# Optimization experiments

Measured on AMD Instinct MI355X. Metric: run time of the kernel, lower is better.

Reference implementation:

```python
import jax, jax.numpy as jnp
import numpy as np
import math

D_MODEL = 1024
NUM_HEADS = 16
D_K = D_MODEL // NUM_HEADS
B, S = 2, 2048


def _linear_weight(key, out_f, in_f):
    return jax.random.normal(key, (out_f, in_f), jnp.float32) * math.sqrt(2.0 / in_f)


def setup_inputs() -> dict:
    key = jax.random.key(0)
    ks = jax.random.split(key, 5)
    x = jax.random.normal(ks[0], (B, S, D_MODEL), jnp.float32)
    return {
        "x": x,
        "Wq": _linear_weight(ks[1], D_MODEL, D_MODEL),
        "bq": jnp.zeros((D_MODEL,), jnp.float32),
        "Wk": _linear_weight(ks[2], D_MODEL, D_MODEL),
        "bk": jnp.zeros((D_MODEL,), jnp.float32),
        "Wv": _linear_weight(ks[3], D_MODEL, D_MODEL),
        "bv": jnp.zeros((D_MODEL,), jnp.float32),
        "Wo": _linear_weight(ks[4], D_MODEL, D_MODEL),
        "bo": jnp.zeros((D_MODEL,), jnp.float32),
    }


def reference(x, Wq, bq, Wk, bk, Wv, bv, Wo, bo):
    b, s, _ = x.shape
    # Projections: x @ W.T + b (CustomLinear stores weight as (out, in))
    q = jnp.einsum("bsd,ed->bse", x, Wq) + bq
    k = jnp.einsum("bsd,ed->bse", x, Wk) + bk
    v = jnp.einsum("bsd,ed->bse", x, Wv) + bv
    # (b, h, s, d_k)
    q = q.reshape(b, s, NUM_HEADS, D_K).transpose(0, 2, 1, 3)
    k = k.reshape(b, s, NUM_HEADS, D_K).transpose(0, 2, 1, 3)
    v = v.reshape(b, s, NUM_HEADS, D_K).transpose(0, 2, 1, 3)
    # Scaled dot-product attention with fully materialized scores (faithful)
    scores = jnp.einsum("bhqd,bhkd->bhqk", q, k) / math.sqrt(D_K)
    attn = jax.nn.softmax(scores, axis=-1)
    out = jnp.einsum("bhqk,bhkd->bhqd", attn, v)
    out = out.transpose(0, 2, 1, 3).reshape(b, s, D_MODEL)
    return jnp.einsum("bsd,ed->bse", out, Wo) + bo
```

## Files before the change

### kernel.cpp

```cpp
#include <hip/hip_runtime.h>
#include <hip/hip_bf16.h>

using bf16 = __hip_bfloat16;
typedef __attribute__((ext_vector_type(8))) short short8;
typedef __attribute__((ext_vector_type(4))) short s4v;
typedef __attribute__((ext_vector_type(4))) float float4v;
typedef __attribute__((ext_vector_type(4))) float f32x4;
typedef __attribute__((ext_vector_type(16))) float f32x16;
typedef __attribute__((ext_vector_type(4))) int i32x4;

#define MFMA16(a, b, c) __builtin_amdgcn_mfma_f32_16x16x32_bf16((a), (b), (c), 0, 0, 0)
#define MFMA32(a, b, c) __builtin_amdgcn_mfma_f32_32x32x16_bf16((a), (b), (c), 0, 0, 0)

#define GLD_LDS16(g, l)                                            \
    __builtin_amdgcn_global_load_lds(                              \
        (const __attribute__((address_space(1))) void*)(g),        \
        (__attribute__((address_space(3))) void*)(l), 16, 0, 0)

constexpr int Bc = 2;
constexpr int Sc = 2048;
constexpr int Hc = 16;
constexpr int DKc = 64;
constexpr int Dc = 1024;
constexpr size_t MEG = 1024 * 1024;

union BFU { bf16 h; short s; };
union PKU { i32x4 i; short8 s; };

__device__ inline short bfbits(float f) {
    BFU u; u.h = __float2bfloat16(f); return u.s;
}

__device__ inline float bits2f(short s) {
    BFU u; u.s = s; return __bfloat162float(u.h);
}

__device__ inline unsigned cvtpk(float a, float b) {
    unsigned r;
    asm("v_cvt_pk_bf16_f32 %0, %1, %2" : "=v"(r) : "v"(a), "v"(b));
    return r;
}

__device__ inline short8 load_cvt8(const float* __restrict__ p) {
    f32x4 a = *(const f32x4*)p;
    f32x4 b = *(const f32x4*)(p + 4);
    short8 r;
    r[0] = bfbits(a[0]); r[1] = bfbits(a[1]); r[2] = bfbits(a[2]); r[3] = bfbits(a[3]);
    r[4] = bfbits(b[0]); r[5] = bfbits(b[1]); r[6] = bfbits(b[2]); r[7] = bfbits(b[3]);
    return r;
}

__global__ __launch_bounds__(256) void cvt_kernel(
    const float* __restrict__ x, const float* __restrict__ Wq,
    const float* __restrict__ Wk, const float* __restrict__ Wv,
    const float* __restrict__ Wo, bf16* __restrict__ dst)
{
    const size_t i = ((size_t)blockIdx.x * 256 + threadIdx.x) * 8;
    const float* s;
    if      (i < 4 * MEG) s = x  + i;
    else if (i < 5 * MEG) s = Wq + (i - 4 * MEG);
    else if (i < 6 * MEG) s = Wk + (i - 5 * MEG);
    else if (i < 7 * MEG) s = Wv + (i - 6 * MEG);
    else                  s = Wo + (i - 7 * MEG);
    *(short8*)(dst + i) = load_cvt8(s);
}

__global__ __launch_bounds__(256) void qkv_gemm_kernel(
    const bf16* __restrict__ x,
    const bf16* __restrict__ Wq, const float* __restrict__ bq,
    const bf16* __restrict__ Wk, const float* __restrict__ bk,
    const bf16* __restrict__ Wv, const float* __restrict__ bv,
    bf16* __restrict__ q_ws, bf16* __restrict__ k_ws, bf16* __restrict__ v_ws)
{
    constexpr int BM = 128, BN = 128, BK = 32;
    __shared__ __align__(16) bf16 sA[BM * BK];
    __shared__ __align__(16) bf16 sB[BN * BK];

    const int bx = blockIdx.x;
    const int sel = bx >> 3;
    const int n0 = (bx & 7) * BN;
    const int m0 = blockIdx.y * BM;

    const bf16* __restrict__ Wsel = (sel == 0) ? Wq : ((sel == 1) ? Wk : Wv);
    const float* __restrict__ bsel = (sel == 0) ? bq : ((sel == 1) ? bk : bv);

    const int t = threadIdx.x;
    const int lane = t & 63;
    const int wave = t >> 6;
    const int ln = lane & 15;
    const int qd = lane >> 4;
    const int wm = (wave >> 1) * 64;
    const int wn = (wave & 1) * 64;

    const int gr = lane >> 2;
    const int gc = (lane & 3) * 8;

    float4v acc[4][4];
#pragma unroll
    for (int i = 0; i < 4; i++)
#pragma unroll
        for (int j = 0; j < 4; j++) acc[i][j] = (float4v)0.0f;

    for (int kk = 0; kk < Dc; kk += BK) {
        __syncthreads();
#pragma unroll
        for (int cc = 0; cc < 2; cc++) {
            const int c = wave * 2 + cc;
            GLD_LDS16(x    + (size_t)(m0 + c * 16 + gr) * Dc + kk + gc, &sA[c * 512]);
            GLD_LDS16(Wsel + (size_t)(n0 + c * 16 + gr) * Dc + kk + gc, &sB[c * 512]);
        }
        __syncthreads();

        short8 af[4], wf[4];
#pragma unroll
        for (int i = 0; i < 4; i++)
            af[i] = *(const short8*)&sA[(wm + i * 16 + ln) * BK + qd * 8];
#pragma unroll
        for (int j = 0; j < 4; j++)
            wf[j] = *(const short8*)&sB[(wn + j * 16 + ln) * BK + qd * 8];
#pragma unroll
        for (int i = 0; i < 4; i++)
#pragma unroll
            for (int j = 0; j < 4; j++)
                acc[i][j] = MFMA16(af[i], wf[j], acc[i][j]);
    }

    constexpr float QSCALE = 0.125f * 1.44269504088896f;

#pragma unroll
    for (int j = 0; j < 4; j++) {
        const int n = n0 + wn + j * 16 + ln;
        const float bias = bsel[n];
        const int h_ = n >> 6, d_ = n & 63;
#pragma unroll
        for (int i = 0; i < 4; i++) {
            const int mbase = m0 + wm + i * 16 + qd * 4;
            const int b_ = mbase >> 11, s0_ = mbase & 2047;
            if (sel == 2) {
                const int dv_ = d_ >> 5, cV = d_ & 31;
                const int ktg = s0_ >> 6, ksl = (s0_ >> 4) & 3;
                const int hiV = (s0_ >> 3) & 1, i0 = s0_ & 7;
                s4v pk;
#pragma unroll
                for (int r = 0; r < 4; r++)
                    pk[r] = bfbits(acc[i][j][r] + bias);
                *(s4v*)&v_ws[(size_t)(b_ * Hc + h_) * Sc * DKc + ktg * 4096
                             + (dv_ * 4 + ksl) * 512 + (cV + 32 * hiV) * 8 + i0] = pk;
            } else if (sel == 1) {
                const int ks_ = d_ >> 4, hiK = (d_ >> 3) & 1, ii = d_ & 7;
#pragma unroll
                for (int r = 0; r < 4; r++) {
                    const int s_ = s0_ + r;
                    const int ktg = s_ >> 6, kv = (s_ >> 5) & 1, cK = s_ & 31;
                    k_ws[(size_t)(b_ * Hc + h_) * Sc * DKc + ktg * 4096
                         + (kv * 4 + ks_) * 512 + (cK + 32 * hiK) * 8 + ii] =
                        __float2bfloat16(acc[i][j][r] + bias);
                }
            } else {
#pragma unroll
                for (int r = 0; r < 4; r++) {
                    const int s_ = s0_ + r;
                    q_ws[(((size_t)(b_ * Hc + h_)) * Sc + s_) * DKc + d_] =
                        __float2bfloat16((acc[i][j][r] + bias) * QSCALE);
                }
            }
        }
    }
}

__global__ __launch_bounds__(256, 4) void attn_kernel(
    const bf16* __restrict__ q_ws, const bf16* __restrict__ kf_ws,
    const bf16* __restrict__ vf_ws, bf16* __restrict__ po0,
    bf16* __restrict__ po1, float* __restrict__ l_ws)
{
    constexpr int NKT = 16;
    __shared__ __align__(16) bf16 sK[2][8 * 512];
    __shared__ __align__(16) bf16 sV[2][8 * 512];

    const int bh = blockIdx.x;
    const int qt = blockIdx.y;
    const int sp = blockIdx.z;
    const int t = threadIdx.x;
    const int lane = t & 63;
    const int wave = t >> 6;
    const int c = lane & 31;
    const int hi = lane >> 5;

    const bf16* __restrict__ Qbase = q_ws + (size_t)bh * Sc * DKc
                                   + (size_t)(qt * 128 + wave * 32) * DKc;
    const bf16* __restrict__ KF = kf_ws + ((size_t)bh * Sc + sp * 1024) * DKc;
    const bf16* __restrict__ VF = vf_ws + ((size_t)bh * Sc + sp * 1024) * DKc;

    short8 qf[4];
#pragma unroll
    for (int ks = 0; ks < 4; ks++)
        qf[ks] = *(const short8*)(Qbase + (size_t)c * DKc + ks * 16 + hi * 8);

    short8 ones8;
    {
        const short ob = (c == 0) ? (short)0x3F80 : (short)0;
#pragma unroll
        for (int i = 0; i < 8; i++) ones8[i] = ob;
    }

    auto stage = [&](int buf, int kt2) {
#pragma unroll
        for (int cc = 0; cc < 4; cc++) {
            const int cid = (wave << 2) + cc;
            if (cid < 8)
                GLD_LDS16(KF + (size_t)kt2 * 4096 + cid * 512 + lane * 8,
                          &sK[buf][cid * 512]);
            else
                GLD_LDS16(VF + (size_t)kt2 * 4096 + (cid - 8) * 512 + lane * 8,
                          &sV[buf][(cid - 8) * 512]);
        }
    };

    f32x16 oacc0 = (f32x16)0.0f;
    f32x16 oacc1 = (f32x16)0.0f;
    f32x16 den   = (f32x16)0.0f;

    stage(0, 0);

    for (int kt = 0; kt < NKT; kt++) {
        const int cur = kt & 1;
        __syncthreads();
        if (kt + 1 < NKT) stage(cur ^ 1, kt + 1);

#pragma unroll
        for (int kv = 0; kv < 2; kv++) {
            f32x16 sacc = (f32x16)0.0f;
            __builtin_amdgcn_s_setprio(1);
#pragma unroll
            for (int ks = 0; ks < 4; ks++) {
                const short8 kfr = *(const short8*)
                    &sK[cur][(kv * 4 + ks) * 512 + lane * 8];
                sacc = MFMA32(kfr, qf[ks], sacc);
            }
            __builtin_amdgcn_s_setprio(0);

            unsigned s0[4][2], sw[4][2];
#pragma unroll
            for (int q = 0; q < 4; q++)
#pragma unroll
                for (int j = 0; j < 2; j++)
                    s0[q][j] = cvtpk(exp2f(sacc[q * 4 + j * 2]),
                                     exp2f(sacc[q * 4 + j * 2 + 1]));
#pragma unroll
            for (int q = 0; q < 4; q++)
#pragma unroll
                for (int j = 0; j < 2; j++)
                    sw[q][j] = (unsigned)__shfl_xor((int)s0[q][j], 32, 64);

            __builtin_amdgcn_s_setprio(1);
#pragma unroll
            for (int m = 0; m < 2; m++) {
                PKU u;
                u.i[0] = (int)(hi ? sw[2 * m + 1][0] : s0[2 * m][0]);
                u.i[1] = (int)(hi ? sw[2 * m + 1][1] : s0[2 * m][1]);
                u.i[2] = (int)(hi ? s0[2 * m + 1][0] : sw[2 * m][0]);
                u.i[3] = (int)(hi ? s0[2 * m + 1][1] : sw[2 * m][1]);
                const short8 ap = u.s;
                const int ksl = kv * 2 + m;
                const short8 vf0 = *(const short8*)
                    &sV[cur][(0 + ksl) * 512 + lane * 8];
                const short8 vf1 = *(const short8*)
                    &sV[cur][(4 + ksl) * 512 + lane * 8];
                oacc0 = MFMA32(ap, vf0, oacc0);
                oacc1 = MFMA32(ap, vf1, oacc1);
                den   = MFMA32(ap, ones8, den);
            }
            __builtin_amdgcn_s_setprio(0);
        }
    }

    const int b_ = bh >> 4, h_ = bh & 15;
    bf16* __restrict__ po = sp ? po1 : po0;
    if (c == 0) {
#pragma unroll
        for (int r = 0; r < 16; r++) {
            const int qrow = (r & 3) + 8 * (r >> 2) + 4 * hi;
            l_ws[(size_t)(sp * 32 + bh) * Sc + qt * 128 + wave * 32 + qrow] =
                den[r];
        }
    }
#pragma unroll
    for (int r = 0; r < 16; r++) {
        const float l = __shfl(den[r], lane & 32, 64);
        const float inv = 1.0f / l;
        const int qrow = (r & 3) + 8 * (r >> 2) + 4 * hi;
        const int s_ = qt * 128 + wave * 32 + qrow;
        const size_t rowb = (((size_t)(b_ * Sc + s_)) * Hc + h_) * DKc;
        po[rowb + c]      = __float2bfloat16(oacc0[r] * inv);
        po[rowb + 32 + c] = __float2bfloat16(oacc1[r] * inv);
    }
}

__global__ __launch_bounds__(256) void combine_kernel(
    bf16* po0, const bf16* __restrict__ po1, const float* __restrict__ l_ws)
{
    const size_t gid = (size_t)blockIdx.x * 256 + threadIdx.x;
    const size_t e = gid * 8;
    const int flat = (int)(e >> 6);
    const int h_ = flat & 15;
    const int bs = flat >> 4;
    const int b_ = bs >> 11, s_ = bs & 2047;
    const int bh = b_ * Hc + h_;
    const float l0 = l_ws[(size_t)bh * Sc + s_];
    const float l1 = l_ws[(size_t)(32 + bh) * Sc + s_];
    const float inv = 1.0f / (l0 + l1);
    const float w0 = l0 * inv, w1 = l1 * inv;
    const short8 a = *(const short8*)(po0 + e);
    const short8 b = *(const short8*)(po1 + e);
    short8 o;
#pragma unroll
    for (int i = 0; i < 8; i++)
        o[i] = bfbits(bits2f(a[i]) * w0 + bits2f(b[i]) * w1);
    *(short8*)(po0 + e) = o;
}

__global__ __launch_bounds__(256) void out_gemm_kernel(
    const bf16* __restrict__ A, const bf16* __restrict__ Wo,
    const float* __restrict__ bo, float* __restrict__ out)
{
    constexpr int BM = 128, BN = 128, BK = 32;
    __shared__ __align__(16) bf16 sA[BM * BK];
    __shared__ __align__(16) bf16 sB[BN * BK];

    const int n0 = blockIdx.x * BN;
    const int m0 = blockIdx.y * BM;

    const int t = threadIdx.x;
    const int lane = t & 63;
    const int wave = t >> 6;
    const int ln = lane & 15;
    const int qd = lane >> 4;
    const int wm = (wave >> 1) * 64;
    const int wn = (wave & 1) * 64;

    const int gr = lane >> 2;
    const int gc = (lane & 3) * 8;

    float4v acc[4][4];
#pragma unroll
    for (int i = 0; i < 4; i++)
#pragma unroll
        for (int j = 0; j < 4; j++) acc[i][j] = (float4v)0.0f;

    for (int kk = 0; kk < Dc; kk += BK) {
        __syncthreads();
#pragma unroll
        for (int cc = 0; cc < 2; cc++) {
            const int c = wave * 2 + cc;
            GLD_LDS16(A  + (size_t)(m0 + c * 16 + gr) * Dc + kk + gc, &sA[c * 512]);
            GLD_LDS16(Wo + (size_t)(n0 + c * 16 + gr) * Dc + kk + gc, &sB[c * 512]);
        }
        __syncthreads();

        short8 af[4], wf[4];
#pragma unroll
        for (int i = 0; i < 4; i++)
            af[i] = *(const short8*)&sA[(wm + i * 16 + ln) * BK + qd * 8];
#pragma unroll
        for (int j = 0; j < 4; j++)
            wf[j] = *(const short8*)&sB[(wn + j * 16 + ln) * BK + qd * 8];
#pragma unroll
        for (int i = 0; i < 4; i++)
#pragma unroll
            for (int j = 0; j < 4; j++)
                acc[i][j] = MFMA16(af[i], wf[j], acc[i][j]);
    }

#pragma unroll
    for (int j = 0; j < 4; j++) {
        const int n = n0 + wn + j * 16 + ln;
        const float bias = bo[n];
#pragma unroll
        for (int i = 0; i < 4; i++) {
            const int mbase = m0 + wm + i * 16 + qd * 4;
#pragma unroll
            for (int r = 0; r < 4; r++) {
                const int m = mbase + r;
                out[(size_t)m * Dc + n] = acc[i][j][r] + bias;
            }
        }
    }
}

extern "C" void kernel_launch(void* const* d_in, const int* in_sizes, int n_in,
                              void* d_out, int out_size, void* d_ws, size_t ws_size,
                              hipStream_t stream)
{
    const float* x  = (const float*)d_in[0];
    const float* Wq = (const float*)d_in[1];
    const float* bq = (const float*)d_in[2];
    const float* Wk = (const float*)d_in[3];
    const float* bk = (const float*)d_in[4];
    const float* Wv = (const float*)d_in[5];
    const float* bv = (const float*)d_in[6];
    const float* Wo = (const float*)d_in[7];
    const float* bo = (const float*)d_in[8];
    float* out = (float*)d_out;

    bf16* base  = (bf16*)d_ws;
    bf16* q_ws  = base;
    bf16* k_ws  = base + 4 * MEG;
    bf16* v_ws  = base + 8 * MEG;
    bf16* ao_ws = base + 12 * MEG;
    bf16* xb    = base + 16 * MEG;
    bf16* po1   = xb;
    bf16* wqb   = base + 20 * MEG;
    float* l_ws = (float*)wqb;
    bf16* wkb   = base + 21 * MEG;
    bf16* wvb   = base + 22 * MEG;
    bf16* wob   = base + 23 * MEG;

    cvt_kernel<<<dim3(4096), 256, 0, stream>>>(x, Wq, Wk, Wv, Wo, xb);
    qkv_gemm_kernel<<<dim3(24, 32), 256, 0, stream>>>(
        xb, wqb, bq, wkb, bk, wvb, bv, q_ws, k_ws, v_ws);
    attn_kernel<<<dim3(32, 16, 2), 256, 0, stream>>>(
        q_ws, k_ws, v_ws, ao_ws, po1, l_ws);
    combine_kernel<<<dim3(2048), 256, 0, stream>>>(ao_ws, po1, l_ws);
    out_gemm_kernel<<<dim3(8, 32), 256, 0, stream>>>(ao_ws, wob, bo, out);
}
```

Measured before the change: 211.6 us.

## Fuse split-KV combine into output projection GEMM A-tile load

Removes the separate combine kernel. The output GEMM now reads both partial attention outputs and their softmax denominators, forms the weighted sum in registers while staging the A tile into shared memory, and prefetches the next A chunk. The N tile is halved to 64 so the grid doubles, which adds parallelism. In exchange, each block redoes the combine for its rows: A traffic doubles and is repeated across 16 column blocks, and the A loads now go through registers instead of direct global-to-LDS copies.

```diff
diff --git a/kernel.cpp b/kernel.cpp
--- a/kernel.cpp
+++ b/kernel.cpp
@@ -296,34 +296,12 @@
     }
 }
 
-__global__ __launch_bounds__(256) void combine_kernel(
-    bf16* po0, const bf16* __restrict__ po1, const float* __restrict__ l_ws)
-{
-    const size_t gid = (size_t)blockIdx.x * 256 + threadIdx.x;
-    const size_t e = gid * 8;
-    const int flat = (int)(e >> 6);
-    const int h_ = flat & 15;
-    const int bs = flat >> 4;
-    const int b_ = bs >> 11, s_ = bs & 2047;
-    const int bh = b_ * Hc + h_;
-    const float l0 = l_ws[(size_t)bh * Sc + s_];
-    const float l1 = l_ws[(size_t)(32 + bh) * Sc + s_];
-    const float inv = 1.0f / (l0 + l1);
-    const float w0 = l0 * inv, w1 = l1 * inv;
-    const short8 a = *(const short8*)(po0 + e);
-    const short8 b = *(const short8*)(po1 + e);
-    short8 o;
-#pragma unroll
-    for (int i = 0; i < 8; i++)
-        o[i] = bfbits(bits2f(a[i]) * w0 + bits2f(b[i]) * w1);
-    *(short8*)(po0 + e) = o;
-}
-
 __global__ __launch_bounds__(256) void out_gemm_kernel(
-    const bf16* __restrict__ A, const bf16* __restrict__ Wo,
+    const bf16* __restrict__ po0, const bf16* __restrict__ po1,
+    const float* __restrict__ l_ws, const bf16* __restrict__ Wo,
     const float* __restrict__ bo, float* __restrict__ out)
 {
-    constexpr int BM = 128, BN = 128, BK = 32;
+    constexpr int BM = 128, BN = 64, BK = 32;
     __shared__ __align__(16) bf16 sA[BM * BK];
     __shared__ __align__(16) bf16 sB[BN * BK];
 
@@ -336,43 +314,74 @@
     const int ln = lane & 15;
     const int qd = lane >> 4;
     const int wm = (wave >> 1) * 64;
-    const int wn = (wave & 1) * 64;
+    const int wn = (wave & 1) * 32;
 
     const int gr = lane >> 2;
     const int gc = (lane & 3) * 8;
 
-    float4v acc[4][4];
+    const int ar = t >> 2;
+    const int ac = (t & 3) * 8;
+
+    float4v acc[4][2];
 #pragma unroll
     for (int i = 0; i < 4; i++)
 #pragma unroll
-        for (int j = 0; j < 4; j++) acc[i][j] = (float4v)0.0f;
+        for (int j = 0; j < 2; j++) acc[i][j] = (float4v)0.0f;
+
+    short8 a0[2], a1[2];
+    auto loadA = [&](int kk) {
+#pragma unroll
+        for (int L = 0; L < 2; L++) {
+            const size_t row = (size_t)(m0 + L * 64 + ar);
+            a0[L] = *(const short8*)&po0[row * Dc + kk + ac];
+            a1[L] = *(const short8*)&po1[row * Dc + kk + ac];
+        }
+    };
+    loadA(0);
 
     for (int kk = 0; kk < Dc; kk += BK) {
         __syncthreads();
-#pragma unroll
-        for (int cc = 0; cc < 2; cc++) {
-            const int c = wave * 2 + cc;
-            GLD_LDS16(A  + (size_t)(m0 + c * 16 + gr) * Dc + kk + gc, &sA[c * 512]);
-            GLD_LDS16(Wo + (size_t)(n0 + c * 16 + gr) * Dc + kk + gc, &sB[c * 512]);
+        GLD_LDS16(Wo + (size_t)(n0 + wave * 16 + gr) * Dc + kk + gc,
+                  &sB[wave * 512]);
+        const short8 c0_0 = a0[0], c0_1 = a0[1];
+        const short8 c1_0 = a1[0], c1_1 = a1[1];
+        if (kk + BK < Dc) loadA(kk + BK);
+        const int h = kk >> 6;
+#pragma unroll
+        for (int L = 0; L < 2; L++) {
+            const int row = m0 + L * 64 + ar;
+            const int b_ = row >> 11, s_ = row & 2047;
+            const int bhl = b_ * Hc + h;
+            const float l0 = l_ws[(size_t)bhl * Sc + s_];
+            const float l1 = l_ws[(size_t)(32 + bhl) * Sc + s_];
+            const float inv = 1.0f / (l0 + l1);
+            const float w0 = l0 * inv, w1 = l1 * inv;
+            const short8 ca = L ? c0_1 : c0_0;
+            const short8 cb = L ? c1_1 : c1_0;
+            short8 o;
+#pragma unroll
+            for (int e = 0; e < 8; e++)
+                o[e] = bfbits(bits2f(ca[e]) * w0 + bits2f(cb[e]) * w1);
+            *(short8*)&sA[(L * 64 + ar) * BK + ac] = o;
         }
         __syncthreads();
 
-        short8 af[4], wf[4];
+        short8 af[4], wf[2];
 #pragma unroll
         for (int i = 0; i < 4; i++)
             af[i] = *(const short8*)&sA[(wm + i * 16 + ln) * BK + qd * 8];
 #pragma unroll
-        for (int j = 0; j < 4; j++)
+        for (int j = 0; j < 2; j++)
             wf[j] = *(const short8*)&sB[(wn + j * 16 + ln) * BK + qd * 8];
 #pragma unroll
         for (int i = 0; i < 4; i++)
 #pragma unroll
-            for (int j = 0; j < 4; j++)
+            for (int j = 0; j < 2; j++)
                 acc[i][j] = MFMA16(af[i], wf[j], acc[i][j]);
     }
 
 #pragma unroll
-    for (int j = 0; j < 4; j++) {
+    for (int j = 0; j < 2; j++) {
         const int n = n0 + wn + j * 16 + ln;
         const float bias = bo[n];
 #pragma unroll
@@ -420,6 +429,6 @@
         xb, wqb, bq, wkb, bk, wvb, bv, q_ws, k_ws, v_ws);
     attn_kernel<<<dim3(32, 16, 2), 256, 0, stream>>>(
         q_ws, k_ws, v_ws, ao_ws, po1, l_ws);
-    combine_kernel<<<dim3(2048), 256, 0, stream>>>(ao_ws, po1, l_ws);
-    out_gemm_kernel<<<dim3(8, 32), 256, 0, stream>>>(ao_ws, wob, bo, out);
-}
+    out_gemm_kernel<<<dim3(16, 32), 256, 0, stream>>>(
+        ao_ws, po1, l_ws, wob, bo, out);
+}
```

After: 225.8 us. +6.7%, slower.
